# Optimization experiments

Measured on AMD Instinct MI355X. Metric: run time of the kernel, lower is better.

## Reference

```python
import jax, jax.numpy as jnp
import numpy as np

N_NODES = 256
HID = 128
ALPHA = 0.01  # LeakyReLU negative slope in GraphAttentionLayer


def _gat(x_flat, W, a):
    """GraphAttentionLayer forward (dropout omitted / eval-deterministic).
    x_flat: (bs, HID) with bs = B*N_NODES. W: (HID, HID), a: (2*HID, 1).
    e[b,i,j] = leakyrelu(a1.h_i + a2.h_j); softmax over j; elu(att @ h).
    """
    h = x_flat.reshape(-1, N_NODES, HID) @ W          # (B, N, H)
    f1 = h @ a[:HID]                                   # (B, N, 1) -> a . h_i
    f2 = h @ a[HID:]                                   # (B, N, 1) -> a . h_j
    e = f1 + jnp.swapaxes(f2, 1, 2)                    # (B, N, N)
    e = jnp.where(e > 0, e, ALPHA * e)                 # LeakyReLU
    att = jax.nn.softmax(e, axis=-1)
    hp = att @ h                                       # (B, N, H)
    return jax.nn.elu(hp).reshape(x_flat.shape)


def setup_inputs() -> dict:
    key = jax.random.key(0)
    ks = iter(jax.random.split(key, 40))
    B, T = 32, 16
    stdv = 1.0 / np.sqrt(HID)

    def u(shape):
        return jax.random.uniform(next(ks), shape, jnp.float32, -stdv, stdv)

    inp = {"x": jax.random.normal(next(ks), (B * N_NODES, T, HID), jnp.float32)}
    for g in ("i", "f", "c", "o"):
        inp[f"W{g}_W"] = u((HID, HID))
        inp[f"W{g}_a"] = u((2 * HID, 1))
        inp[f"U{g}_W"] = u((HID, HID))
        inp[f"U{g}_a"] = u((2 * HID, 1))
        inp[f"b_{g}"] = u((HID,))
    inp["pool_w"] = u((1, N_NODES))
    inp["pool_b"] = u((1,))
    inp["linh_w"] = u((HID, HID))
    inp["linh_b"] = u((HID,))
    inp["linq_w"] = u((HID, HID))
    inp["linq_b"] = u((HID,))
    inp["linu_w"] = u((1, HID))
    inp["linu_b"] = u((1,))
    return inp


def _f_att(h_flat, pool_w, pool_b, linh_w, linh_b, linq_w, linq_b, linu_w, linu_b):
    h = h_flat.reshape(-1, N_NODES, HID)               # (B, N, H)
    # pool over nodes: (B,H,N) @ (N,1) -> (B,H)
    q = jax.nn.relu(jnp.einsum('bnh,n->bh', h, pool_w[0]) + pool_b)
    q = q[:, None, :]                                  # (B, 1, H), broadcasts over N
    t = jnp.tanh(h @ linh_w.T + linh_b + q @ linq_w.T + linq_b)
    a = jax.nn.sigmoid(t @ linu_w.T + linu_b)          # (B, N, 1)
    return (h * a).reshape(h_flat.shape)


def reference(x, Wi_W, Wi_a, Ui_W, Ui_a, Wf_W, Wf_a, Uf_W, Uf_a,
              Wc_W, Wc_a, Uc_W, Uc_a, Wo_W, Wo_a, Uo_W, Uo_a,
              b_i, b_f, b_c, b_o,
              pool_w, pool_b, linh_w, linh_b, linq_w, linq_b, linu_w, linu_b):
    bs, T, _ = x.shape
    h0 = jnp.zeros((bs, HID), x.dtype)
    c0 = jnp.zeros((bs, HID), x.dtype)

    def step(carry, x_t):
        h, c = carry
        i_t = jax.nn.sigmoid(_gat(x_t, Wi_W, Wi_a) + _gat(h, Ui_W, Ui_a) + b_i)
        f_t = jax.nn.sigmoid(_gat(x_t, Wf_W, Wf_a) + _gat(h, Uf_W, Uf_a) + b_f)
        g_t = jnp.tanh(_gat(x_t, Wc_W, Wc_a) + _gat(h, Uc_W, Uc_a) + b_c)
        o_t = jax.nn.sigmoid(_gat(x_t, Wo_W, Wo_a) + _gat(h, Uo_W, Uo_a) + b_o)
        c_new = f_t * c + i_t * g_t
        h_new = o_t * jnp.tanh(c_new)
        h_new = _f_att(h_new, pool_w, pool_b, linh_w, linh_b,
                       linq_w, linq_b, linu_w, linu_b) + h_new
        return (h_new, c_new), h_new

    (h_t, c_t), hs = jax.lax.scan(step, (h0, c0), jnp.swapaxes(x, 0, 1))
    # torch: cat(list of (bs,H), dim=0) -> (T*bs, H); transpose(0,1) -> (H, T*bs)
    hidden_seq = hs.reshape(T * bs, HID).T
    return hidden_seq, (h_t, c_t)
```

## Files before the change

### kernel.cpp

```cpp
#include <hip/hip_runtime.h>
#include <cstdint>
#include <cstddef>

#define NN   256
#define HIDD 128
#define NB   32
#define TT   16
#define BSZ  (NB*NN)

struct GP {
  const float* W[8];
  const float* A[8];
};

typedef __attribute__((ext_vector_type(8))) short bf16x8;
typedef __attribute__((ext_vector_type(4))) float f32x4;
typedef _Float16 f16x8 __attribute__((ext_vector_type(8)));

__device__ __forceinline__ uint16_t bf16rn(float f) {
  uint32_t u = __float_as_uint(f);
  uint32_t r = u + 0x7fffu + ((u >> 16) & 1u);
  return (uint16_t)(r >> 16);
}
__device__ __forceinline__ float bf16f(uint16_t h) {
  return __uint_as_float((uint32_t)h << 16);
}
__device__ __forceinline__ uint16_t f16b(float f) {
  union { _Float16 h; uint16_t u; } cv;
  cv.h = (_Float16)f;
  return cv.u;
}
__device__ __forceinline__ float fsig(float x) {
  return 1.f/(1.f + __expf(-x));
}
__device__ __forceinline__ float ftanh(float x) {
  float xc = fmaxf(-44.f, fminf(44.f, x));
  float e = __expf(-2.f*xc);
  return (1.f - e)/(1.f + e);
}

__global__ __launch_bounds__(256) void k0_convw(GP gp, uint4* __restrict__ WfH,
    uint4* __restrict__ WfL)
{
  const int s = blockIdx.x;
  const float* __restrict__ W = gp.W[s];
  const int tid = threadIdx.x;
  #pragma unroll
  for (int it = 0; it < 8; ++it) {
    int f = it*256 + tid;
    int cf = f >> 8, ks = (f >> 6) & 3, l = f & 63;
    int col = cf*16 + (l & 15);
    int kbase = (ks*4 + (l >> 4))*8;
    float v[8];
    #pragma unroll
    for (int j = 0; j < 8; ++j) v[j] = W[(kbase + j)*HIDD + col];
    uint32_t uh[4], ul[4];
    #pragma unroll
    for (int j = 0; j < 4; ++j) {
      uint16_t h0 = bf16rn(v[2*j]), h1 = bf16rn(v[2*j+1]);
      uint16_t l0 = bf16rn(v[2*j]   - bf16f(h0));
      uint16_t l1 = bf16rn(v[2*j+1] - bf16f(h1));
      uh[j] = (uint32_t)h0 | ((uint32_t)h1 << 16);
      ul[j] = (uint32_t)l0 | ((uint32_t)l1 << 16);
    }
    WfH[s*2048 + f] = make_uint4(uh[0], uh[1], uh[2], uh[3]);
    WfL[s*2048 + f] = make_uint4(ul[0], ul[1], ul[2], ul[3]);
  }
}

__global__ __launch_bounds__(256) void k0_lh(const float* __restrict__ lhw,
    uint4* __restrict__ LhH, uint4* __restrict__ LhL)
{
  const int tid = threadIdx.x;
  #pragma unroll
  for (int it = 0; it < 8; ++it) {
    int f = it*256 + tid;
    int cf = f >> 8, ks = (f >> 6) & 3, l = f & 63;
    int col = cf*16 + (l & 15);
    int kbase = (ks*4 + (l >> 4))*8;
    float v[8];
    #pragma unroll
    for (int j = 0; j < 8; ++j) v[j] = lhw[col*HIDD + kbase + j];
    uint32_t uh[4], ul[4];
    #pragma unroll
    for (int j = 0; j < 4; ++j) {
      uint16_t h0 = bf16rn(v[2*j]), h1 = bf16rn(v[2*j+1]);
      uint16_t l0 = bf16rn(v[2*j]   - bf16f(h0));
      uint16_t l1 = bf16rn(v[2*j+1] - bf16f(h1));
      uh[j] = (uint32_t)h0 | ((uint32_t)h1 << 16);
      ul[j] = (uint32_t)l0 | ((uint32_t)l1 << 16);
    }
    LhH[f] = make_uint4(uh[0], uh[1], uh[2], uh[3]);
    LhL[f] = make_uint4(ul[0], ul[1], ul[2], ul[3]);
  }
}

__global__ __launch_bounds__(128) void k0_wa(GP gp, float* __restrict__ Wa)
{
  const int s = blockIdx.x, k = threadIdx.x;
  const float* __restrict__ W = gp.W[s];
  const float* __restrict__ A = gp.A[s];
  float d1 = 0.f, d2 = 0.f;
  #pragma unroll 4
  for (int c = 0; c < HIDD; ++c) {
    float wv = W[k*HIDD + c];
    d1 += wv*A[c];
    d2 += wv*A[HIDD + c];
  }
  Wa[s*256 + k]       = d1;
  Wa[s*256 + 128 + k] = d2;
}

template<int NG>
__global__ __launch_bounds__(256) void k1_gemm(const float* __restrict__ x,
    const float* __restrict__ hstate, const uint4* __restrict__ WfH,
    const uint4* __restrict__ WfL, const float* __restrict__ Wa,
    uint4* __restrict__ HfO, float* __restrict__ f12,
    int sBase, int wside, int tArg)
{
  const int t = wside ? blockIdx.y : tArg;
  const int s0 = wside ? 0 : (sBase + blockIdx.y*NG);
  const int row0 = blockIdx.x * 64;
  const int b = row0 >> 8;
  const int kc = (row0 >> 6) & 3;
  const int tid = threadIdx.x, lane = tid & 63, w = tid >> 6;
  __shared__ __align__(16) uint4 AH[1024];
  __shared__ __align__(16) uint4 AL[1024];
  __shared__ __align__(16) char  ThB[128*144];
  __shared__ float red1[4][64], red2[4][64];
  const bool useX = wside || (s0 < 4);

  #pragma unroll
  for (int it = 0; it < 4; ++it) {
    int linear = it*256 + tid;
    int r = linear >> 4, blk = linear & 15;
    const float4* p = useX
      ? reinterpret_cast<const float4*>(x + (size_t)(row0 + r)*(TT*HIDD) + (size_t)t*HIDD)
      : reinterpret_cast<const float4*>(hstate + (size_t)(row0 + r)*HIDD);
    float4 v0 = p[blk*2], v1 = p[blk*2 + 1];
    float vv[8] = {v0.x, v0.y, v0.z, v0.w, v1.x, v1.y, v1.z, v1.w};
    uint32_t uh[4], ul[4];
    #pragma unroll
    for (int j = 0; j < 4; ++j) {
      uint16_t h0 = bf16rn(vv[2*j]), h1 = bf16rn(vv[2*j+1]);
      uint16_t l0 = bf16rn(vv[2*j]   - bf16f(h0));
      uint16_t l1 = bf16rn(vv[2*j+1] - bf16f(h1));
      uh[j] = (uint32_t)h0 | ((uint32_t)h1 << 16);
      ul[j] = (uint32_t)l0 | ((uint32_t)l1 << 16);
    }
    int dst = r*16 + (blk ^ (r & 7));
    AH[dst] = make_uint4(uh[0], uh[1], uh[2], uh[3]);
    AL[dst] = make_uint4(ul[0], ul[1], ul[2], ul[3]);
  }
  __syncthreads();

  const int kg = lane >> 4;
  bf16x8 ah[4], al[4];
  {
    int i = w*16 + (lane & 15);
    #pragma unroll
    for (int ks = 0; ks < 4; ++ks) {
      int blk = (ks*4 + kg) ^ (i & 7);
      ah[ks] = *reinterpret_cast<const bf16x8*>(&AH[i*16 + blk]);
      al[ks] = *reinterpret_cast<const bf16x8*>(&AL[i*16 + blk]);
    }
  }
  const int frow = tid & 63, kq = tid >> 6;

  #pragma unroll 1
  for (int gi = 0; gi < NG; ++gi) {
    const int s = wside ? gi : (s0 + gi);
    const int tIdx = wside ? (t*4 + gi) : (s - sBase);
    {
      const float* __restrict__ wa = Wa + s*256;
      float d1 = 0.f, d2 = 0.f;
      #pragma unroll
      for (int bb = 0; bb < 4; ++bb) {
        int bi = kq*4 + bb;
        uint4 vh = AH[frow*16 + (bi ^ (frow & 7))];
        uint4 vl = AL[frow*16 + (bi ^ (frow & 7))];
        #pragma unroll
        for (int j = 0; j < 4; ++j) {
          uint32_t uh = (&vh.x)[j], ul2 = (&vl.x)[j];
          float e0 = __uint_as_float(uh << 16) + __uint_as_float(ul2 << 16);
          float e1 = __uint_as_float(uh & 0xffff0000u) + __uint_as_float(ul2 & 0xffff0000u);
          int k0 = bi*8 + j*2;
          d1 += e0*wa[k0]     + e1*wa[k0+1];
          d2 += e0*wa[128+k0] + e1*wa[128+k0+1];
        }
      }
      red1[kq][frow] = d1; red2[kq][frow] = d2;
    }
    f32x4 acc[8];
    #pragma unroll
    for (int c = 0; c < 8; ++c) acc[c] = (f32x4){0.f, 0.f, 0.f, 0.f};
    const uint4* __restrict__ BH = WfH + s*2048;
    const uint4* __restrict__ BL = WfL + s*2048;
    #pragma unroll
    for (int cf = 0; cf < 8; ++cf) {
      bf16x8 bh[4], bl[4];
      #pragma unroll
      for (int ks = 0; ks < 4; ++ks) {
        bh[ks] = *reinterpret_cast<const bf16x8*>(&BH[(cf*4 + ks)*64 + lane]);
        bl[ks] = *reinterpret_cast<const bf16x8*>(&BL[(cf*4 + ks)*64 + lane]);
      }
      #pragma unroll
      for (int ks = 0; ks < 4; ++ks) {
        acc[cf] = __builtin_amdgcn_mfma_f32_16x16x32_bf16(ah[ks], bh[ks], acc[cf], 0, 0, 0);
        acc[cf] = __builtin_amdgcn_mfma_f32_16x16x32_bf16(al[ks], bh[ks], acc[cf], 0, 0, 0);
        acc[cf] = __builtin_amdgcn_mfma_f32_16x16x32_bf16(ah[ks], bl[ks], acc[cf], 0, 0, 0);
      }
    }
    __syncthreads();
    if (tid < 64) {
      float* fb = f12 + (size_t)tIdx*2*BSZ;
      fb[row0 + tid]       = red1[0][tid] + red1[1][tid] + red1[2][tid] + red1[3][tid];
      fb[BSZ + row0 + tid] = red2[0][tid] + red2[1][tid] + red2[2][tid] + red2[3][tid];
    }
    {
      int jlb = w*16 + (lane >> 4)*4;
      #pragma unroll
      for (int cf = 0; cf < 8; ++cf) {
        int col = cf*16 + (lane & 15);
        uint16_t hh[4];
        #pragma unroll
        for (int ii = 0; ii < 4; ++ii) hh[ii] = f16b(acc[cf][ii]);
        *reinterpret_cast<uint2*>(ThB + col*144 + jlb*2) =
            make_uint2((uint32_t)hh[0] | ((uint32_t)hh[1] << 16),
                       (uint32_t)hh[2] | ((uint32_t)hh[3] << 16));
      }
    }
    __syncthreads();
    uint4* __restrict__ Hf = HfO + (size_t)(tIdx*NB + b)*4096;
    #pragma unroll
    for (int it = 0; it < 4; ++it) {
      int fl = it*256 + tid;
      int l2 = fl & 63, cf = (fl >> 6) & 7, ks = fl >> 9;
      int col = cf*16 + (l2 & 15);
      int jl = ks*32 + (l2 >> 4)*8;
      uint4 v = *reinterpret_cast<const uint4*>(ThB + col*144 + jl*2);
      size_t fg = (size_t)((kc*2 + ks)*8 + cf)*64 + l2;
      Hf[fg] = v;
    }
  }
}

__global__ __launch_bounds__(256) void k2_attn(
    const uint4* __restrict__ HfW, const uint4* __restrict__ HfU,
    const float* __restrict__ f12W, const float* __restrict__ f12U,
    float* __restrict__ gat, int t, int pre)
{
  const int s = blockIdx.y;
  const int b = blockIdx.x;
  const int roff = blockIdx.z * 64;
  const int tid = threadIdx.x, lane = tid & 63, w = tid >> 6;
  const int rl = tid & 63, qh = tid >> 6;
  __shared__ __align__(16) float f2L[NN];
  __shared__ __align__(16) float sums[256];
  __shared__ __align__(16) uint16_t Pb[64*64];
  const uint4 *BH;
  const float* fb;
  if (pre && s < 4) {
    size_t tg = (size_t)(t*4 + s);
    BH = HfW + (tg*NB + b)*4096;
    fb = f12W + tg*2*BSZ;
  } else {
    size_t tg = (size_t)(s - (pre ? 4 : 0));
    BH = HfU + (tg*NB + b)*4096;
    fb = f12U + tg*2*BSZ;
  }
  f2L[tid] = fb[BSZ + b*NN + tid];
  const float f1v = fb[b*NN + roff + rl];

  const float4* f24 = reinterpret_cast<const float4*>(f2L);
  float ssum = 0.f;
  f32x4 acc[8];
  #pragma unroll
  for (int c = 0; c < 8; ++c) acc[c] = (f32x4){0.f, 0.f, 0.f, 0.f};
  char* PbB = reinterpret_cast<char*>(Pb);
  const int kg = lane >> 4;

  for (int kc = 0; kc < 4; ++kc) {
    __syncthreads();
    #pragma unroll
    for (int bb = 0; bb < 2; ++bb) {
      int blk = qh*2 + bb;
      float4 va = f24[kc*16 + blk*2];
      float4 vb = f24[kc*16 + blk*2 + 1];
      float e0 = f1v + va.x; e0 = e0 > 0.f ? e0 : 0.01f*e0;
      float e1 = f1v + va.y; e1 = e1 > 0.f ? e1 : 0.01f*e1;
      float e2 = f1v + va.z; e2 = e2 > 0.f ? e2 : 0.01f*e2;
      float e3 = f1v + va.w; e3 = e3 > 0.f ? e3 : 0.01f*e3;
      float e4 = f1v + vb.x; e4 = e4 > 0.f ? e4 : 0.01f*e4;
      float e5 = f1v + vb.y; e5 = e5 > 0.f ? e5 : 0.01f*e5;
      float e6 = f1v + vb.z; e6 = e6 > 0.f ? e6 : 0.01f*e6;
      float e7 = f1v + vb.w; e7 = e7 > 0.f ? e7 : 0.01f*e7;
      float p0 = __expf(e0), p1 = __expf(e1), p2 = __expf(e2), p3 = __expf(e3);
      float p4 = __expf(e4), p5 = __expf(e5), p6 = __expf(e6), p7 = __expf(e7);
      ssum += (p0 + p1) + (p2 + p3) + ((p4 + p5) + (p6 + p7));
      uint32_t u0 = (uint32_t)f16b(p0) | ((uint32_t)f16b(p1) << 16);
      uint32_t u1 = (uint32_t)f16b(p2) | ((uint32_t)f16b(p3) << 16);
      uint32_t u2 = (uint32_t)f16b(p4) | ((uint32_t)f16b(p5) << 16);
      uint32_t u3 = (uint32_t)f16b(p6) | ((uint32_t)f16b(p7) << 16);
      *reinterpret_cast<uint4*>(PbB + rl*128 + ((blk ^ (rl & 7)) << 4)) =
          make_uint4(u0, u1, u2, u3);
    }
    __syncthreads();
    #pragma unroll
    for (int ks = 0; ks < 2; ++ks) {
      int i = w*16 + (lane & 15);
      int blk = (ks*4 + kg) ^ (i & 7);
      f16x8 af = *reinterpret_cast<const f16x8*>(PbB + i*128 + blk*16);
      #pragma unroll
      for (int c = 0; c < 8; ++c) {
        size_t fg = (size_t)((kc*2 + ks)*8 + c)*64 + lane;
        f16x8 bh = *reinterpret_cast<const f16x8*>(&BH[fg]);
        acc[c] = __builtin_amdgcn_mfma_f32_16x16x32_f16(af, bh, acc[c], 0, 0, 0);
      }
    }
  }
  sums[tid] = ssum;
  __syncthreads();

  float* __restrict__ gout = gat + ((size_t)s*BSZ + (size_t)b*NN)*HIDD;
  {
    int lrb = w*16 + (lane >> 4)*4;
    int row = roff + lrb;
    #pragma unroll
    for (int ii = 0; ii < 4; ++ii) {
      float rs = 1.f / (sums[lrb + ii] + sums[64 + lrb + ii] +
                        sums[128 + lrb + ii] + sums[192 + lrb + ii]);
      #pragma unroll
      for (int c = 0; c < 8; ++c) {
        int col = c*16 + (lane & 15);
        float v = acc[c][ii] * rs;
        v = v > 0.f ? v : (__expf(v) - 1.f);
        gout[(size_t)(row + ii)*HIDD + col] = v;
      }
    }
  }
}

__global__ __launch_bounds__(256) void k3_gates(const float4* __restrict__ gat4,
    const float4* __restrict__ bi4, const float4* __restrict__ bf4,
    const float4* __restrict__ bc4, const float4* __restrict__ bo4,
    float4* __restrict__ c4, float4* __restrict__ hm4, float4* __restrict__ outc4,
    const float* __restrict__ pw, float4* __restrict__ qpart)
{
  const size_t S4 = (size_t)BSZ*HIDD/4;
  const int tid = threadIdx.x;
  size_t idx = (size_t)blockIdx.x*256 + tid;
  int hc = (int)(idx & 31);
  float4 gi = gat4[idx], gf = gat4[S4+idx], gc = gat4[2*S4+idx], go = gat4[3*S4+idx];
  float4 ui = gat4[4*S4+idx], uf = gat4[5*S4+idx], uc = gat4[6*S4+idx], uo = gat4[7*S4+idx];
  float4 Bi = bi4[hc], Bf = bf4[hc], Bc = bc4[hc], Bo = bo4[hc];
  float4 cv = c4[idx], hv, cn;
  #pragma unroll
  for (int j = 0; j < 4; ++j) {
    float xi = (&gi.x)[j] + (&ui.x)[j] + (&Bi.x)[j];
    float xf = (&gf.x)[j] + (&uf.x)[j] + (&Bf.x)[j];
    float xc = (&gc.x)[j] + (&uc.x)[j] + (&Bc.x)[j];
    float xo = (&go.x)[j] + (&uo.x)[j] + (&Bo.x)[j];
    float it = fsig(xi);
    float ft = fsig(xf);
    float gt = ftanh(xc);
    float ot = fsig(xo);
    float c = ft*(&cv.x)[j] + it*gt;
    (&cn.x)[j] = c;
    (&hv.x)[j] = ot*ftanh(c);
  }
  c4[idx] = cn;
  hm4[idx] = hv;
  if (outc4) outc4[idx] = cn;
  int row = (int)(idx >> 5);
  float pwv = pw[row & 255];
  __shared__ float4 pp[256];
  pp[tid] = make_float4(hv.x*pwv, hv.y*pwv, hv.z*pwv, hv.w*pwv);
  __syncthreads();
  if (tid < 32) {
    float4 sa = pp[tid];
    #pragma unroll
    for (int k = 1; k < 8; ++k) {
      float4 v = pp[tid + k*32];
      sa.x += v.x; sa.y += v.y; sa.z += v.z; sa.w += v.w;
    }
    qpart[(size_t)blockIdx.x*32 + tid] = sa;
  }
}

__global__ __launch_bounds__(256) void k5_fatt(const float* __restrict__ hmid,
    const float* __restrict__ qpartF, const float* __restrict__ pb,
    const float* __restrict__ lqw, const float* __restrict__ lqb,
    const float* __restrict__ lhb, const uint4* __restrict__ LhH,
    const uint4* __restrict__ LhL, const float* __restrict__ luw,
    const float* __restrict__ lub,
    float* __restrict__ hstate, float* __restrict__ out, int t,
    float* __restrict__ outh)
{
  const int tid = threadIdx.x, lane = tid & 63, w = tid >> 6;
  const int row0 = blockIdx.x * 64;
  const int b = row0 >> 8;
  __shared__ __align__(16) uint4 SH[2048];
  __shared__ float otile[HIDD][65];
  __shared__ float qsum[HIDD];
  __shared__ float qqL[HIDD];
  uint4* AH = SH;
  uint4* AL = SH + 1024;

  #pragma unroll
  for (int it = 0; it < 4; ++it) {
    int linear = it*256 + tid;
    int r = linear >> 4, blk = linear & 15;
    const float4* p = reinterpret_cast<const float4*>(hmid + (size_t)(row0 + r)*HIDD);
    float4 v0 = p[blk*2], v1 = p[blk*2 + 1];
    float vv[8] = {v0.x, v0.y, v0.z, v0.w, v1.x, v1.y, v1.z, v1.w};
    uint32_t uh[4], ul[4];
    #pragma unroll
    for (int j = 0; j < 4; ++j) {
      uint16_t h0 = bf16rn(vv[2*j]), h1 = bf16rn(vv[2*j+1]);
      uint16_t l0 = bf16rn(vv[2*j]   - bf16f(h0));
      uint16_t l1 = bf16rn(vv[2*j+1] - bf16f(h1));
      uh[j] = (uint32_t)h0 | ((uint32_t)h1 << 16);
      ul[j] = (uint32_t)l0 | ((uint32_t)l1 << 16);
    }
    int dst = r*16 + (blk ^ (r & 7));
    AH[dst] = make_uint4(uh[0], uh[1], uh[2], uh[3]);
    AL[dst] = make_uint4(ul[0], ul[1], ul[2], ul[3]);
  }
  if (tid < 128) {
    const float* qp = qpartF + (size_t)b*4096;
    float q = 0.f;
    #pragma unroll 8
    for (int p = 0; p < 32; ++p) q += qp[p*128 + tid];
    qsum[tid] = fmaxf(q + pb[0], 0.f);
  }
  __syncthreads();
  const int kg = lane >> 4;
  bf16x8 ah[4], al[4];
  {
    int i = w*16 + (lane & 15);
    #pragma unroll
    for (int ks = 0; ks < 4; ++ks) {
      int blk = (ks*4 + kg) ^ (i & 7);
      ah[ks] = *reinterpret_cast<const bf16x8*>(&AH[i*16 + blk]);
      al[ks] = *reinterpret_cast<const bf16x8*>(&AL[i*16 + blk]);
    }
  }
  if (tid < 128) {
    float acc = 0.f;
    #pragma unroll 4
    for (int k = 0; k < HIDD; ++k) acc += qsum[k]*lqw[tid*HIDD + k];
    qqL[tid] = acc + lqb[tid] + lhb[tid];
  }
  __syncthreads();

  f32x4 acc[8];
  #pragma unroll
  for (int c = 0; c < 8; ++c) acc[c] = (f32x4){0.f, 0.f, 0.f, 0.f};
  #pragma unroll
  for (int cf = 0; cf < 8; ++cf) {
    bf16x8 bh[4], bl[4];
    #pragma unroll
    for (int ks = 0; ks < 4; ++ks) {
      bh[ks] = *reinterpret_cast<const bf16x8*>(&LhH[(cf*4 + ks)*64 + lane]);
      bl[ks] = *reinterpret_cast<const bf16x8*>(&LhL[(cf*4 + ks)*64 + lane]);
    }
    #pragma unroll
    for (int ks = 0; ks < 4; ++ks) {
      acc[cf] = __builtin_amdgcn_mfma_f32_16x16x32_bf16(ah[ks], bh[ks], acc[cf], 0, 0, 0);
      acc[cf] = __builtin_amdgcn_mfma_f32_16x16x32_bf16(al[ks], bh[ks], acc[cf], 0, 0, 0);
      acc[cf] = __builtin_amdgcn_mfma_f32_16x16x32_bf16(ah[ks], bl[ks], acc[cf], 0, 0, 0);
    }
  }

  float apv[4] = {0.f, 0.f, 0.f, 0.f};
  #pragma unroll
  for (int cf = 0; cf < 8; ++cf) {
    int col = cf*16 + (lane & 15);
    float lu = luw[col];
    float qv = qqL[col];
    #pragma unroll
    for (int ii = 0; ii < 4; ++ii)
      apv[ii] += ftanh(acc[cf][ii] + qv) * lu;
  }
  #pragma unroll
  for (int off = 1; off < 16; off <<= 1) {
    #pragma unroll
    for (int ii = 0; ii < 4; ++ii)
      apv[ii] += __shfl_xor(apv[ii], off, 64);
  }
  float lb = lub[0];
  float av[4];
  #pragma unroll
  for (int ii = 0; ii < 4; ++ii)
    av[ii] = 1.f + fsig(apv[ii] + lb);

  #pragma unroll
  for (int cf = 0; cf < 8; ++cf) {
    int col = cf*16 + (lane & 15);
    #pragma unroll
    for (int ii = 0; ii < 4; ++ii) {
      int rloc = w*16 + (lane >> 4)*4 + ii;
      int row = row0 + rloc;
      float h = hmid[(size_t)row*HIDD + col];
      float v = h*av[ii];
      hstate[(size_t)row*HIDD + col] = v;
      if (outh) outh[(size_t)row*HIDD + col] = v;
      otile[col][rloc] = v;
    }
  }
  __syncthreads();
  #pragma unroll
  for (int i = 0; i < 32; ++i) {
    int idx = tid + i*256;
    int h = idx >> 6, rr = idx & 63;
    out[(size_t)h*(TT*(size_t)BSZ) + (size_t)t*BSZ + row0 + rr] = otile[h][rr];
  }
}

extern "C" void kernel_launch(void* const* d_in, const int* in_sizes, int n_in,
                              void* d_out, int out_size, void* d_ws, size_t ws_size,
                              hipStream_t stream)
{
  const float* x = (const float*)d_in[0];
  GP gp;
  int wIdx[8], aIdx[8], bIdx[4];
  bool dictOrder = (in_sizes[5] == HIDD);
  if (dictOrder) {
    for (int g = 0; g < 4; ++g) {
      int base = 1 + 5*g;
      wIdx[g]   = base;     aIdx[g]   = base + 1;
      wIdx[4+g] = base + 2; aIdx[4+g] = base + 3;
      bIdx[g]   = base + 4;
    }
  } else {
    for (int g = 0; g < 4; ++g) {
      int base = 1 + 4*g;
      wIdx[g]   = base;     aIdx[g]   = base + 1;
      wIdx[4+g] = base + 2; aIdx[4+g] = base + 3;
      bIdx[g]   = 17 + g;
    }
  }
  for (int s = 0; s < 8; ++s) {
    gp.W[s] = (const float*)d_in[wIdx[s]];
    gp.A[s] = (const float*)d_in[aIdx[s]];
  }
  const float* bi  = (const float*)d_in[bIdx[0]];
  const float* bf  = (const float*)d_in[bIdx[1]];
  const float* bc  = (const float*)d_in[bIdx[2]];
  const float* bo  = (const float*)d_in[bIdx[3]];
  const float* pw  = (const float*)d_in[21];
  const float* pb  = (const float*)d_in[22];
  const float* lhw = (const float*)d_in[23];
  const float* lhb = (const float*)d_in[24];
  const float* lqw = (const float*)d_in[25];
  const float* lqb = (const float*)d_in[26];
  const float* luw = (const float*)d_in[27];
  const float* lub = (const float*)d_in[28];

  const size_t S = (size_t)BSZ*HIDD;
  float* ws = (float*)d_ws;
  float* gat    = ws;
  float* hstate = gat + 8*S;
  float* cstate = hstate + S;
  float* hmid   = cstate + S;
  float* f12U   = hmid + S;
  float* qpart  = f12U + 131072;
  float* Wa     = qpart + 131072;
  uint4* WfH    = (uint4*)(Wa + 2048);
  uint4* WfL    = WfH + 16384;
  uint4* LhH    = WfL + 16384;
  uint4* LhL    = LhH + 2048;
  uint4* HfU    = LhL + 2048;
  uint4* HfW    = HfU + (size_t)8*NB*4096;
  float* f12W   = (float*)(HfW + (size_t)64*NB*4096);
  bool pre = ws_size >= (size_t)205*1024*1024;

  float* out = (float*)d_out;
  const size_t off = (size_t)HIDD * (size_t)TT * (size_t)BSZ;

  hipMemsetAsync(hstate, 0, S*sizeof(float), stream);
  hipMemsetAsync(cstate, 0, S*sizeof(float), stream);
  k0_convw<<<8, 256, 0, stream>>>(gp, WfH, WfL);
  k0_wa<<<8, 128, 0, stream>>>(gp, Wa);
  k0_lh<<<1, 256, 0, stream>>>(lhw, LhH, LhL);

  if (pre) {
    k1_gemm<4><<<dim3(128, 16), 256, 0, stream>>>(x, hstate, WfH, WfL, Wa,
        HfW, f12W, 0, 1, 0);
  }

  for (int t = 0; t < TT; ++t) {
    bool last = (t == TT - 1);
    if (pre) {
      k1_gemm<1><<<dim3(128, 4), 256, 0, stream>>>(x, hstate, WfH, WfL, Wa,
          HfU, f12U, 4, 0, t);
      k2_attn<<<dim3(NB, 8, 4), 256, 0, stream>>>(HfW, HfU, f12W, f12U, gat, t, 1);
    } else {
      k1_gemm<1><<<dim3(128, 8), 256, 0, stream>>>(x, hstate, WfH, WfL, Wa,
          HfU, f12U, 0, 0, t);
      k2_attn<<<dim3(NB, 8, 4), 256, 0, stream>>>(HfU, HfU, f12U, f12U, gat, t, 0);
    }
    k3_gates<<<1024, 256, 0, stream>>>((const float4*)gat, (const float4*)bi,
        (const float4*)bf, (const float4*)bc, (const float4*)bo,
        (float4*)cstate, (float4*)hmid,
        last ? (float4*)(out + off + S) : (float4*)nullptr,
        pw, (float4*)qpart);
    k5_fatt<<<128, 256, 0, stream>>>(hmid, qpart, pb, lqw, lqb, lhb,
        LhH, LhL, luw, lub, hstate, out, t, last ? (out + off) : nullptr);
  }
}
```

Measured before the change: 1.144 ms.

## Fuse recurrent GEMM with input-side attention and store gate outputs as fp16

Adds a combined kernel that, in the precomputed path, runs the h-state GEMM tiles alongside the attention blocks for the input-side (W) gates, alternating roles by block index. The U-side attention then runs in a smaller follow-up launch. This overlaps independent work and removes one serialization point per step. The GAT outputs are also written as fp16 instead of fp32, halving the gate kernel's read traffic at some cost in precision.

```diff
diff --git a/kernel.cpp b/kernel.cpp
--- a/kernel.cpp
+++ b/kernel.cpp
@@ -29,6 +29,15 @@
   union { _Float16 h; uint16_t u; } cv;
   cv.h = (_Float16)f;
   return cv.u;
+}
+__device__ __forceinline__ float f16f(uint16_t u) {
+  union { uint16_t u; _Float16 h; } cv;
+  cv.u = u;
+  return (float)cv.h;
+}
+__device__ __forceinline__ float h4(uint2 v, int j) {
+  uint32_t u = ((j < 2) ? v.x : v.y) >> ((j & 1)*16);
+  return f16f((uint16_t)u);
 }
 __device__ __forceinline__ float fsig(float x) {
   return 1.f/(1.f + __expf(-x));
@@ -245,33 +254,14 @@
   }
 }
 
-__global__ __launch_bounds__(256) void k2_attn(
-    const uint4* __restrict__ HfW, const uint4* __restrict__ HfU,
-    const float* __restrict__ f12W, const float* __restrict__ f12U,
-    float* __restrict__ gat, int t, int pre)
-{
-  const int s = blockIdx.y;
-  const int b = blockIdx.x;
-  const int roff = blockIdx.z * 64;
-  const int tid = threadIdx.x, lane = tid & 63, w = tid >> 6;
+__device__ __forceinline__ void attn_body(const uint4* __restrict__ BH,
+    const float* __restrict__ fb, uint16_t* __restrict__ goutH,
+    int b, int roff, int tid, uint16_t* Pb, float* f2L, float* sums)
+{
+  const int lane = tid & 63, w = tid >> 6;
   const int rl = tid & 63, qh = tid >> 6;
-  __shared__ __align__(16) float f2L[NN];
-  __shared__ __align__(16) float sums[256];
-  __shared__ __align__(16) uint16_t Pb[64*64];
-  const uint4 *BH;
-  const float* fb;
-  if (pre && s < 4) {
-    size_t tg = (size_t)(t*4 + s);
-    BH = HfW + (tg*NB + b)*4096;
-    fb = f12W + tg*2*BSZ;
-  } else {
-    size_t tg = (size_t)(s - (pre ? 4 : 0));
-    BH = HfU + (tg*NB + b)*4096;
-    fb = f12U + tg*2*BSZ;
-  }
   f2L[tid] = fb[BSZ + b*NN + tid];
   const float f1v = fb[b*NN + roff + rl];
-
   const float4* f24 = reinterpret_cast<const float4*>(f2L);
   float ssum = 0.f;
   f32x4 acc[8];
@@ -322,7 +312,6 @@
   sums[tid] = ssum;
   __syncthreads();
 
-  float* __restrict__ gout = gat + ((size_t)s*BSZ + (size_t)b*NN)*HIDD;
   {
     int lrb = w*16 + (lane >> 4)*4;
     int row = roff + lrb;
@@ -335,32 +324,204 @@
         int col = c*16 + (lane & 15);
         float v = acc[c][ii] * rs;
         v = v > 0.f ? v : (__expf(v) - 1.f);
-        gout[(size_t)(row + ii)*HIDD + col] = v;
-      }
-    }
-  }
-}
-
-__global__ __launch_bounds__(256) void k3_gates(const float4* __restrict__ gat4,
+        goutH[(size_t)(row + ii)*HIDD + col] = f16b(v);
+      }
+    }
+  }
+}
+
+__global__ __launch_bounds__(256) void k12(const float* __restrict__ hstate,
+    const uint4* __restrict__ WfH, const uint4* __restrict__ WfL,
+    const float* __restrict__ Wa, uint4* __restrict__ HfU,
+    float* __restrict__ f12U, const uint4* __restrict__ HfW,
+    const float* __restrict__ f12W, uint16_t* __restrict__ gatH, int t)
+{
+  __shared__ __align__(16) uint4 SH[2048];
+  __shared__ __align__(16) float xtra[512];
+  const int bid = blockIdx.x;
+  const int role = bid & 1, idx = bid >> 1;
+  const int tid = threadIdx.x, lane = tid & 63, w = tid >> 6;
+
+  if (role == 0) {
+    const int xt = idx & 127, g = idx >> 7;
+    const int s = 4 + g;
+    const int row0 = xt * 64;
+    const int b = row0 >> 8, kc = (row0 >> 6) & 3;
+    uint4* AH = SH;
+    uint4* AL = SH + 1024;
+    float (*red1)[64] = reinterpret_cast<float(*)[64]>(xtra);
+    float (*red2)[64] = reinterpret_cast<float(*)[64]>(xtra + 256);
+
+    #pragma unroll
+    for (int it = 0; it < 4; ++it) {
+      int linear = it*256 + tid;
+      int r = linear >> 4, blk = linear & 15;
+      const float4* p = reinterpret_cast<const float4*>(hstate + (size_t)(row0 + r)*HIDD);
+      float4 v0 = p[blk*2], v1 = p[blk*2 + 1];
+      float vv[8] = {v0.x, v0.y, v0.z, v0.w, v1.x, v1.y, v1.z, v1.w};
+      uint32_t uh[4], ul[4];
+      #pragma unroll
+      for (int j = 0; j < 4; ++j) {
+        uint16_t h0 = bf16rn(vv[2*j]), h1 = bf16rn(vv[2*j+1]);
+        uint16_t l0 = bf16rn(vv[2*j]   - bf16f(h0));
+        uint16_t l1 = bf16rn(vv[2*j+1] - bf16f(h1));
+        uh[j] = (uint32_t)h0 | ((uint32_t)h1 << 16);
+        ul[j] = (uint32_t)l0 | ((uint32_t)l1 << 16);
+      }
+      int dst = r*16 + (blk ^ (r & 7));
+      AH[dst] = make_uint4(uh[0], uh[1], uh[2], uh[3]);
+      AL[dst] = make_uint4(ul[0], ul[1], ul[2], ul[3]);
+    }
+    __syncthreads();
+
+    {
+      const int frow = tid & 63, kq = tid >> 6;
+      const float* __restrict__ wa = Wa + s*256;
+      float d1 = 0.f, d2 = 0.f;
+      #pragma unroll
+      for (int bb = 0; bb < 4; ++bb) {
+        int bi = kq*4 + bb;
+        uint4 vh = AH[frow*16 + (bi ^ (frow & 7))];
+        uint4 vl = AL[frow*16 + (bi ^ (frow & 7))];
+        #pragma unroll
+        for (int j = 0; j < 4; ++j) {
+          uint32_t uh = (&vh.x)[j], ul2 = (&vl.x)[j];
+          float e0 = __uint_as_float(uh << 16) + __uint_as_float(ul2 << 16);
+          float e1 = __uint_as_float(uh & 0xffff0000u) + __uint_as_float(ul2 & 0xffff0000u);
+          int k0 = bi*8 + j*2;
+          d1 += e0*wa[k0]     + e1*wa[k0+1];
+          d2 += e0*wa[128+k0] + e1*wa[128+k0+1];
+        }
+      }
+      red1[kq][frow] = d1; red2[kq][frow] = d2;
+    }
+    const int kg = lane >> 4;
+    bf16x8 ah[4], al[4];
+    {
+      int i = w*16 + (lane & 15);
+      #pragma unroll
+      for (int ks = 0; ks < 4; ++ks) {
+        int blk = (ks*4 + kg) ^ (i & 7);
+        ah[ks] = *reinterpret_cast<const bf16x8*>(&AH[i*16 + blk]);
+        al[ks] = *reinterpret_cast<const bf16x8*>(&AL[i*16 + blk]);
+      }
+    }
+    __syncthreads();
+    if (tid < 64) {
+      float* fb = f12U + (size_t)g*2*BSZ;
+      fb[row0 + tid]       = red1[0][tid] + red1[1][tid] + red1[2][tid] + red1[3][tid];
+      fb[BSZ + row0 + tid] = red2[0][tid] + red2[1][tid] + red2[2][tid] + red2[3][tid];
+    }
+
+    f32x4 acc[8];
+    #pragma unroll
+    for (int c = 0; c < 8; ++c) acc[c] = (f32x4){0.f, 0.f, 0.f, 0.f};
+    const uint4* __restrict__ BH = WfH + s*2048;
+    const uint4* __restrict__ BL = WfL + s*2048;
+    #pragma unroll
+    for (int cf = 0; cf < 8; ++cf) {
+      bf16x8 bh[4], bl[4];
+      #pragma unroll
+      for (int ks = 0; ks < 4; ++ks) {
+        bh[ks] = *reinterpret_cast<const bf16x8*>(&BH[(cf*4 + ks)*64 + lane]);
+        bl[ks] = *reinterpret_cast<const bf16x8*>(&BL[(cf*4 + ks)*64 + lane]);
+      }
+      #pragma unroll
+      for (int ks = 0; ks < 4; ++ks) {
+        acc[cf] = __builtin_amdgcn_mfma_f32_16x16x32_bf16(ah[ks], bh[ks], acc[cf], 0, 0, 0);
+        acc[cf] = __builtin_amdgcn_mfma_f32_16x16x32_bf16(al[ks], bh[ks], acc[cf], 0, 0, 0);
+        acc[cf] = __builtin_amdgcn_mfma_f32_16x16x32_bf16(ah[ks], bl[ks], acc[cf], 0, 0, 0);
+      }
+    }
+
+    char* ThB = reinterpret_cast<char*>(SH);
+    {
+      int jlb = w*16 + (lane >> 4)*4;
+      #pragma unroll
+      for (int cf = 0; cf < 8; ++cf) {
+        int col = cf*16 + (lane & 15);
+        uint16_t hh[4];
+        #pragma unroll
+        for (int ii = 0; ii < 4; ++ii) hh[ii] = f16b(acc[cf][ii]);
+        *reinterpret_cast<uint2*>(ThB + col*144 + jlb*2) =
+            make_uint2((uint32_t)hh[0] | ((uint32_t)hh[1] << 16),
+                       (uint32_t)hh[2] | ((uint32_t)hh[3] << 16));
+      }
+    }
+    __syncthreads();
+    uint4* __restrict__ Hf = HfU + (size_t)(g*NB + b)*4096;
+    #pragma unroll
+    for (int it = 0; it < 4; ++it) {
+      int fl = it*256 + tid;
+      int l2 = fl & 63, cf = (fl >> 6) & 7, ks = fl >> 9;
+      int col = cf*16 + (l2 & 15);
+      int jl = ks*32 + (l2 >> 4)*8;
+      uint4 v = *reinterpret_cast<const uint4*>(ThB + col*144 + jl*2);
+      size_t fg = (size_t)((kc*2 + ks)*8 + cf)*64 + l2;
+      Hf[fg] = v;
+    }
+  } else {
+    const int b = idx & 31, g = (idx >> 5) & 3, chunk = idx >> 7;
+    const int roff = chunk*64;
+    size_t tg = (size_t)(t*4 + g);
+    const uint4* BH = HfW + (tg*NB + b)*4096;
+    const float* fb = f12W + tg*2*BSZ;
+    uint16_t* goutH = gatH + ((size_t)g*BSZ + (size_t)b*NN)*HIDD;
+    attn_body(BH, fb, goutH, b, roff, tid,
+              reinterpret_cast<uint16_t*>(SH), xtra, xtra + 256);
+  }
+}
+
+__global__ __launch_bounds__(256) void k2_attn(
+    const uint4* __restrict__ HfW, const uint4* __restrict__ HfU,
+    const float* __restrict__ f12W, const float* __restrict__ f12U,
+    uint16_t* __restrict__ gatH, int t, int pre, int sBase)
+{
+  const int s = sBase + blockIdx.y;
+  const int b = blockIdx.x;
+  const int roff = blockIdx.z * 64;
+  const int tid = threadIdx.x;
+  __shared__ __align__(16) float f2L[NN];
+  __shared__ __align__(16) float sums[256];
+  __shared__ __align__(16) uint16_t Pb[64*64];
+  const uint4 *BH;
+  const float* fb;
+  if (pre && s < 4) {
+    size_t tg = (size_t)(t*4 + s);
+    BH = HfW + (tg*NB + b)*4096;
+    fb = f12W + tg*2*BSZ;
+  } else {
+    size_t tg = (size_t)(s - (pre ? 4 : 0));
+    BH = HfU + (tg*NB + b)*4096;
+    fb = f12U + tg*2*BSZ;
+  }
+  uint16_t* goutH = gatH + ((size_t)s*BSZ + (size_t)b*NN)*HIDD;
+  attn_body(BH, fb, goutH, b, roff, tid, Pb, f2L, sums);
+}
+
+__global__ __launch_bounds__(256) void k3_gates(const uint16_t* __restrict__ gatH,
     const float4* __restrict__ bi4, const float4* __restrict__ bf4,
     const float4* __restrict__ bc4, const float4* __restrict__ bo4,
     float4* __restrict__ c4, float4* __restrict__ hm4, float4* __restrict__ outc4,
     const float* __restrict__ pw, float4* __restrict__ qpart)
 {
-  const size_t S4 = (size_t)BSZ*HIDD/4;
+  const size_t S4h = (size_t)BSZ*HIDD/4;
   const int tid = threadIdx.x;
   size_t idx = (size_t)blockIdx.x*256 + tid;
   int hc = (int)(idx & 31);
-  float4 gi = gat4[idx], gf = gat4[S4+idx], gc = gat4[2*S4+idx], go = gat4[3*S4+idx];
-  float4 ui = gat4[4*S4+idx], uf = gat4[5*S4+idx], uc = gat4[6*S4+idx], uo = gat4[7*S4+idx];
+  const uint2* gH = reinterpret_cast<const uint2*>(gatH);
+  uint2 g0 = gH[idx],          g1 = gH[S4h + idx];
+  uint2 g2 = gH[2*S4h + idx],  g3 = gH[3*S4h + idx];
+  uint2 g4 = gH[4*S4h + idx],  g5 = gH[5*S4h + idx];
+  uint2 g6 = gH[6*S4h + idx],  g7 = gH[7*S4h + idx];
   float4 Bi = bi4[hc], Bf = bf4[hc], Bc = bc4[hc], Bo = bo4[hc];
   float4 cv = c4[idx], hv, cn;
   #pragma unroll
   for (int j = 0; j < 4; ++j) {
-    float xi = (&gi.x)[j] + (&ui.x)[j] + (&Bi.x)[j];
-    float xf = (&gf.x)[j] + (&uf.x)[j] + (&Bf.x)[j];
-    float xc = (&gc.x)[j] + (&uc.x)[j] + (&Bc.x)[j];
-    float xo = (&go.x)[j] + (&uo.x)[j] + (&Bo.x)[j];
+    float xi = h4(g0, j) + h4(g4, j) + (&Bi.x)[j];
+    float xf = h4(g1, j) + h4(g5, j) + (&Bf.x)[j];
+    float xc = h4(g2, j) + h4(g6, j) + (&Bc.x)[j];
+    float xo = h4(g3, j) + h4(g7, j) + (&Bo.x)[j];
     float it = fsig(xi);
     float ft = fsig(xf);
     float gt = ftanh(xc);
@@ -560,8 +721,8 @@
 
   const size_t S = (size_t)BSZ*HIDD;
   float* ws = (float*)d_ws;
-  float* gat    = ws;
-  float* hstate = gat + 8*S;
+  uint16_t* gatH = (uint16_t*)ws;
+  float* hstate = ws + 4*S;
   float* cstate = hstate + S;
   float* hmid   = cstate + S;
   float* f12U   = hmid + S;
@@ -593,15 +754,17 @@
   for (int t = 0; t < TT; ++t) {
     bool last = (t == TT - 1);
     if (pre) {
-      k1_gemm<1><<<dim3(128, 4), 256, 0, stream>>>(x, hstate, WfH, WfL, Wa,
-          HfU, f12U, 4, 0, t);
-      k2_attn<<<dim3(NB, 8, 4), 256, 0, stream>>>(HfW, HfU, f12W, f12U, gat, t, 1);
+      k12<<<1024, 256, 0, stream>>>(hstate, WfH, WfL, Wa, HfU, f12U,
+          HfW, f12W, gatH, t);
+      k2_attn<<<dim3(NB, 4, 4), 256, 0, stream>>>(HfW, HfU, f12W, f12U,
+          gatH, t, 1, 4);
     } else {
       k1_gemm<1><<<dim3(128, 8), 256, 0, stream>>>(x, hstate, WfH, WfL, Wa,
           HfU, f12U, 0, 0, t);
-      k2_attn<<<dim3(NB, 8, 4), 256, 0, stream>>>(HfU, HfU, f12U, f12U, gat, t, 0);
-    }
-    k3_gates<<<1024, 256, 0, stream>>>((const float4*)gat, (const float4*)bi,
+      k2_attn<<<dim3(NB, 8, 4), 256, 0, stream>>>(HfU, HfU, f12U, f12U,
+          gatH, t, 0, 0);
+    }
+    k3_gates<<<1024, 256, 0, stream>>>(gatH, (const float4*)bi,
         (const float4*)bf, (const float4*)bc, (const float4*)bo,
         (float4*)cstate, (float4*)hmid,
         last ? (float4*)(out + off + S) : (float4*)nullptr,
```

Measured after the change: 1.292 ms. 1.13x slower.
